# Performance work log

Hardware: AMD Instinct MI355X
Metric: run time of the kernel (lower is better)

## Reference

```python
import jax, jax.numpy as jnp
import numpy as np

VOCAB = 4096
CODE_DIM = 3
DECAY = 0.99
EPS = 1e-05
BETA = 0.25


def setup_inputs() -> dict:
    key = jax.random.key(0)
    k1, k2, k3, k4 = jax.random.split(key, 4)
    B, L, D = 4, 16384, CODE_DIM
    feats = jax.random.normal(k1, (B, L, D), dtype=jnp.float32)
    embed = jax.random.normal(k2, (VOCAB, D), dtype=jnp.float32) * 0.02  # trunc_normal std=init_gain
    ema_cluster_size = jax.random.uniform(k3, (VOCAB,), dtype=jnp.float32)
    ema_weight = jax.random.normal(k4, (VOCAB, D), dtype=jnp.float32) * 0.02
    return {"feats": feats, "embed": embed,
            "ema_cluster_size": ema_cluster_size, "ema_weight": ema_weight}


def reference(feats, embed, ema_cluster_size, ema_weight):
    B, L, D = feats.shape
    V = embed.shape[0]
    flat = feats.reshape(-1, D)  # (N, D)

    # squared-distance argmin nearest-codebook lookup
    dist = (jnp.sum(flat * flat, axis=1, keepdims=True)
            - 2.0 * flat @ embed.T
            + jnp.sum(embed * embed, axis=1))
    idx = jnp.argmin(dist, axis=1)  # (N,)

    quant = embed[idx].reshape(B, L, D)

    # VQ losses (embedding is frozen in torch; stop_grad for faithful grads)
    e_latent_loss = jnp.mean((quant - jax.lax.stop_gradient(feats)) ** 2)
    commit_loss = BETA * jnp.mean((feats - jax.lax.stop_gradient(quant)) ** 2)
    vq_loss = e_latent_loss + commit_loss

    # EMA codebook update (training branch): scatter-accumulate per code
    ones = jnp.ones_like(idx, dtype=flat.dtype)
    batch_cluster_size = jax.ops.segment_sum(ones, idx, num_segments=V)        # == one_hot.sum(0)
    batch_weight_sum = jax.ops.segment_sum(flat, idx, num_segments=V)          # == one_hot.T @ flat

    new_cluster_size = DECAY * ema_cluster_size + (1.0 - DECAY) * batch_cluster_size
    new_ema_weight = DECAY * ema_weight + (1.0 - DECAY) * batch_weight_sum

    n = jnp.sum(new_cluster_size)
    cluster_size = (new_cluster_size + EPS) / (n + V * EPS) * n
    new_embed = new_ema_weight / cluster_size[:, None]

    # code_dim == 3: renormalize the (cos, sin) columns to unit norm
    cos_sin = new_embed[:, 1:]
    norm = jnp.maximum(jnp.linalg.norm(cos_sin, axis=1, keepdims=True), EPS)
    new_embed = jnp.concatenate([new_embed[:, :1], cos_sin / norm], axis=1)

    # straight-through estimator
    quant_st = feats + jax.lax.stop_gradient(quant - feats)

    return (quant_st, idx.reshape(B, L), vq_loss,
            new_embed, new_cluster_size, new_ema_weight)
```

## Files before the change

kernel.cpp:

```cpp
#include <hip/hip_runtime.h>
#include <math.h>

#define VOCAB 4096
#define NROWS 65536
#define DECAYF 0.99f
#define EPSF 1e-5f

typedef unsigned long long u64;
typedef unsigned int u32;
typedef float vf2 __attribute__((ext_vector_type(2)));


__global__ __launch_bounds__(1024) void vq_scan_kernel(
    const float* __restrict__ feats,
    const float* __restrict__ embed,
    float* __restrict__ quant_out,
    float* __restrict__ idx_out,
    double* __restrict__ errpart,
    double* __restrict__ n_acc) {
    #pragma clang fp contract(off)
    __shared__ float4 tab[VOCAB];

    const int tid  = threadIdx.x;
    const int wave = tid >> 6;
    const int lane = tid & 63;

    if (blockIdx.x == 0 && tid == 0) *n_acc = 0.0;

    #pragma unroll
    for (int k = 0; k < 2; ++k) {
        const int p = tid + k * 1024;
        const float* e = embed + p * 6;
        const float x0 = e[0], y0 = e[1], z0 = e[2];
        const float x1 = e[3], y1 = e[4], z1 = e[5];
        const float s0 = (x0 * x0 + y0 * y0) + z0 * z0;
        const float s1 = (x1 * x1 + y1 * y1) + z1 * z1;
        tab[2 * p]     = make_float4(-2.f * x0, -2.f * x1, -2.f * y0, -2.f * y1);
        tab[2 * p + 1] = make_float4(-2.f * z0, -2.f * z1, s0, s1);
    }

    const int rbase = blockIdx.x * 256 + lane * 4;
    const float4 fa = *(const float4*)(feats + rbase * 3);
    const float4 fb = *(const float4*)(feats + rbase * 3 + 4);
    const float4 fc = *(const float4*)(feats + rbase * 3 + 8);
    const float f0[4] = {fa.x, fa.w, fb.z, fc.y};
    const float f1[4] = {fa.y, fb.x, fb.w, fc.z};
    const float f2[4] = {fa.z, fb.y, fc.x, fc.w};
    vf2 f0s[4], f1s[4], f2s[4], fss[4];
    #pragma unroll
    for (int r = 0; r < 4; ++r) {
        const float fs = (f0[r] * f0[r] + f1[r] * f1[r]) + f2[r] * f2[r];
        f0s[r] = (vf2){f0[r], f0[r]};
        f1s[r] = (vf2){f1[r], f1[r]};
        f2s[r] = (vf2){f2[r], f2[r]};
        fss[r] = (vf2){fs, fs};
    }

    __syncthreads();

    float best[4] = {INFINITY, INFINITY, INFINITY, INFINITY};
    int   bj[4]   = {0, 0, 0, 0};
    const float4* __restrict__ wt = tab + (wave << 8);
    const int cw = wave << 8;

    #pragma unroll 2
    for (int i = 0; i < 128; ++i) {
        const float4 A = wt[2 * i];
        const float4 B = wt[2 * i + 1];
        const vf2 xs = (vf2){A.x, A.y};
        const vf2 ys = (vf2){A.z, A.w};
        const vf2 zs = (vf2){B.x, B.y};
        const vf2 es = (vf2){B.z, B.w};
        const int c0 = cw + 2 * i;
        #pragma unroll
        for (int r = 0; r < 4; ++r) {
            vf2 t = __builtin_elementwise_fma(zs, f2s[r],
                      __builtin_elementwise_fma(ys, f1s[r], xs * f0s[r]));
            vf2 d = (fss[r] + t) + es;
            if (d.x < best[r]) { best[r] = d.x; bj[r] = c0; }
            if (d.y < best[r]) { best[r] = d.y; bj[r] = c0 + 1; }
        }
    }

    u64 key[4];
    #pragma unroll
    for (int r = 0; r < 4; ++r) {
        const u32 b  = __float_as_uint(best[r]);
        const u32 mb = b ^ ((u32)((int)b >> 31) | 0x80000000u);
        key[r] = ((u64)mb << 32) | (u32)bj[r];
    }

    __syncthreads();
    u64* mk = (u64*)tab;
    if (wave != 0) {
        #pragma unroll
        for (int r = 0; r < 4; ++r)
            mk[(wave * 4 + r) * 64 + lane] = key[r];
    }
    __syncthreads();
    if (wave == 0) {
        for (int w = 1; w < 16; ++w) {
            #pragma unroll
            for (int r = 0; r < 4; ++r) {
                const u64 k = mk[(w * 4 + r) * 64 + lane];
                key[r] = k < key[r] ? k : key[r];
            }
        }
        int cand[4];
        #pragma unroll
        for (int r = 0; r < 4; ++r) cand[r] = (int)(u32)key[r];

        *(float4*)(idx_out + rbase) =
            make_float4((float)cand[0], (float)cand[1], (float)cand[2], (float)cand[3]);

        float q[4][3];
        #pragma unroll
        for (int r = 0; r < 4; ++r) {
            q[r][0] = embed[cand[r] * 3 + 0];
            q[r][1] = embed[cand[r] * 3 + 1];
            q[r][2] = embed[cand[r] * 3 + 2];
        }
        *(float4*)(quant_out + rbase * 3)     = make_float4(q[0][0], q[0][1], q[0][2], q[1][0]);
        *(float4*)(quant_out + rbase * 3 + 4) = make_float4(q[1][1], q[1][2], q[2][0], q[2][1]);
        *(float4*)(quant_out + rbase * 3 + 8) = make_float4(q[2][2], q[3][0], q[3][1], q[3][2]);

        float err = 0.0f;
        #pragma unroll
        for (int r = 0; r < 4; ++r) {
            const float d0 = q[r][0] - f0[r], d1 = q[r][1] - f1[r], d2 = q[r][2] - f2[r];
            err += d0 * d0 + d1 * d1 + d2 * d2;
        }
        #pragma unroll
        for (int off = 32; off >= 1; off >>= 1) err += __shfl_xor(err, off);
        if (lane == 0) errpart[blockIdx.x] = (double)err;
    }
}

__global__ __launch_bounds__(1024) void seg_kernel(
    const float* __restrict__ feats,
    const float* __restrict__ idx_f,
    float4* __restrict__ part,
    int iters) {
    __shared__ float lcnt[VOCAB];
    __shared__ float lw[VOCAB * 3];
    const int t = threadIdx.x;
    const int b = blockIdx.x;

    #pragma unroll
    for (int i = 0; i < 4; ++i)  lcnt[t + i * 1024] = 0.0f;
    #pragma unroll
    for (int i = 0; i < 12; ++i) lw[t + i * 1024] = 0.0f;
    __syncthreads();

    const int base = b * iters * 1024;
    for (int i = 0; i < iters; ++i) {
        const int row = base + i * 1024 + t;
        const int cand = (int)idx_f[row];
        atomicAdd(&lcnt[cand], 1.0f);
        atomicAdd(&lw[cand * 3 + 0], feats[row * 3 + 0]);
        atomicAdd(&lw[cand * 3 + 1], feats[row * 3 + 1]);
        atomicAdd(&lw[cand * 3 + 2], feats[row * 3 + 2]);
    }
    __syncthreads();

    #pragma unroll
    for (int i = 0; i < 4; ++i) {
        const int v = t + i * 1024;
        part[b * VOCAB + v] = make_float4(lcnt[v], lw[3 * v], lw[3 * v + 1], lw[3 * v + 2]);
    }
}

__global__ __launch_bounds__(256) void ema_reduce_kernel(
    const float4* __restrict__ part,
    const float* __restrict__ ema_cs,
    const float* __restrict__ ema_w,
    const double* __restrict__ errpart,
    float* __restrict__ ncs_out,
    float* __restrict__ nw_out,
    double* __restrict__ n_acc,
    float* __restrict__ loss_out,
    int nseg) {
    const int v = blockIdx.x * 256 + threadIdx.x;
    float c = 0.f, w0 = 0.f, w1 = 0.f, w2 = 0.f;
    for (int b = 0; b < nseg; ++b) {
        const float4 p = part[b * VOCAB + v];
        c += p.x; w0 += p.y; w1 += p.z; w2 += p.w;
    }
    const float ncs = DECAYF * ema_cs[v] + (1.0f - DECAYF) * c;
    ncs_out[v] = ncs;
    nw_out[v * 3 + 0] = DECAYF * ema_w[v * 3 + 0] + (1.0f - DECAYF) * w0;
    nw_out[v * 3 + 1] = DECAYF * ema_w[v * 3 + 1] + (1.0f - DECAYF) * w1;
    nw_out[v * 3 + 2] = DECAYF * ema_w[v * 3 + 2] + (1.0f - DECAYF) * w2;

    double nloc = (double)ncs;
    #pragma unroll
    for (int off = 32; off >= 1; off >>= 1) nloc += __shfl_xor(nloc, off);
    if ((threadIdx.x & 63) == 0) atomicAdd(n_acc, nloc);

    if (blockIdx.x == 0) {
        __shared__ double se[256];
        const int t = threadIdx.x;
        se[t] = errpart[t];
        __syncthreads();
        #pragma unroll
        for (int s = 128; s > 0; s >>= 1) {
            if (t < s) se[t] += se[t + s];
            __syncthreads();
        }
        if (t == 0)
            loss_out[0] = (float)(1.25 * se[0] / (double)(NROWS * 3));
    }
}

__global__ __launch_bounds__(256) void final_kernel(
    const float* __restrict__ ncs,
    const float* __restrict__ nw,
    const double* __restrict__ n_acc,
    float* __restrict__ embed_out) {
    const int v = blockIdx.x * 256 + threadIdx.x;
    const float n = (float)(*n_acc);
    const float cs = (ncs[v] + EPSF) / (n + (float)VOCAB * EPSF) * n;
    const float d0 = nw[v * 3 + 0] / cs;
    const float d1 = nw[v * 3 + 1] / cs;
    const float d2 = nw[v * 3 + 2] / cs;
    const float nrm = fmaxf(sqrtf(d1 * d1 + d2 * d2), EPSF);
    embed_out[v * 3 + 0] = d0;
    embed_out[v * 3 + 1] = d1 / nrm;
    embed_out[v * 3 + 2] = d2 / nrm;
}

extern "C" void kernel_launch(void* const* d_in, const int* in_sizes, int n_in,
                              void* d_out, int out_size, void* d_ws, size_t ws_size,
                              hipStream_t stream) {
    const float* feats  = (const float*)d_in[0];
    const float* embed  = (const float*)d_in[1];
    const float* ema_cs = (const float*)d_in[2];
    const float* ema_w  = (const float*)d_in[3];

    float* out = (float*)d_out;
    float* quant_out = out;
    float* idx_out   = out + 196608;
    float* loss_out  = out + 262144;
    float* embed_out = out + 262145;
    float* ncs_out   = out + 274433;
    float* nw_out    = out + 278529;

    char* wsb = (char*)d_ws;
    double* errpart = (double*)wsb;
    double* n_ac    = (double*)(wsb + 2048);
    float4* part    = (float4*)(wsb + 4096);

    const size_t per_seg = (size_t)VOCAB * 16;
    const size_t avail = ws_size > 4096 ? ws_size - 4096 : 0;
    int nseg = 8;
    if (avail >= 64 * per_seg)      nseg = 64;
    else if (avail >= 32 * per_seg) nseg = 32;
    else if (avail >= 16 * per_seg) nseg = 16;
    const int iters = NROWS / (nseg * 1024);

    vq_scan_kernel<<<NROWS / 256, 1024, 0, stream>>>(feats, embed,
                                                     quant_out, idx_out,
                                                     errpart, n_ac);
    seg_kernel<<<nseg, 1024, 0, stream>>>(feats, idx_out, part, iters);
    ema_reduce_kernel<<<VOCAB / 256, 256, 0, stream>>>(part, ema_cs, ema_w,
                                                       errpart, ncs_out, nw_out,
                                                       n_ac, loss_out, nseg);
    final_kernel<<<VOCAB / 256, 256, 0, stream>>>(ncs_out, nw_out, n_ac, embed_out);
}
```

Before: 80.02 us.

## Group argmin scan by eight codes, compute n analytically, fuse final kernel

The distance scan now takes a min over groups of eight codes and records only the group base. It then recomputes those eight distances to recover the exact first-minimum index, which cuts compare/select work in the hot loop. The total n is computed from the sum of ema_cluster_size plus the known row count, moved into an extra seg_kernel block, so the final kernel can be folded into the EMA reduce kernel. This drops one launch and the double atomics, at the cost of changing n's summation order and precision from double to float.

```diff
diff --git a/kernel.cpp b/kernel.cpp
--- a/kernel.cpp
+++ b/kernel.cpp
@@ -11,21 +11,18 @@
 typedef float vf2 __attribute__((ext_vector_type(2)));
 
 
-__global__ __launch_bounds__(1024) void vq_scan_kernel(
+__global__ __launch_bounds__(1024, 4) void vq_scan_kernel(
     const float* __restrict__ feats,
     const float* __restrict__ embed,
     float* __restrict__ quant_out,
     float* __restrict__ idx_out,
-    double* __restrict__ errpart,
-    double* __restrict__ n_acc) {
+    double* __restrict__ errpart) {
     #pragma clang fp contract(off)
     __shared__ float4 tab[VOCAB];
 
     const int tid  = threadIdx.x;
     const int wave = tid >> 6;
     const int lane = tid & 63;
-
-    if (blockIdx.x == 0 && tid == 0) *n_acc = 0.0;
 
     #pragma unroll
     for (int k = 0; k < 2; ++k) {
@@ -59,35 +56,57 @@
     __syncthreads();
 
     float best[4] = {INFINITY, INFINITY, INFINITY, INFINITY};
-    int   bj[4]   = {0, 0, 0, 0};
+    int   gb[4]   = {0, 0, 0, 0};
     const float4* __restrict__ wt = tab + (wave << 8);
     const int cw = wave << 8;
 
-    #pragma unroll 2
-    for (int i = 0; i < 128; ++i) {
-        const float4 A = wt[2 * i];
-        const float4 B = wt[2 * i + 1];
-        const vf2 xs = (vf2){A.x, A.y};
-        const vf2 ys = (vf2){A.z, A.w};
-        const vf2 zs = (vf2){B.x, B.y};
-        const vf2 es = (vf2){B.z, B.w};
-        const int c0 = cw + 2 * i;
+    for (int g = 0; g < 32; ++g) {
+        const float4 A0 = wt[8 * g + 0], B0 = wt[8 * g + 1];
+        const float4 A1 = wt[8 * g + 2], B1 = wt[8 * g + 3];
+        const float4 A2 = wt[8 * g + 4], B2 = wt[8 * g + 5];
+        const float4 A3 = wt[8 * g + 6], B3 = wt[8 * g + 7];
+        const vf2 xs0 = {A0.x, A0.y}, ys0 = {A0.z, A0.w}, zs0 = {B0.x, B0.y}, es0 = {B0.z, B0.w};
+        const vf2 xs1 = {A1.x, A1.y}, ys1 = {A1.z, A1.w}, zs1 = {B1.x, B1.y}, es1 = {B1.z, B1.w};
+        const vf2 xs2 = {A2.x, A2.y}, ys2 = {A2.z, A2.w}, zs2 = {B2.x, B2.y}, es2 = {B2.z, B2.w};
+        const vf2 xs3 = {A3.x, A3.y}, ys3 = {A3.z, A3.w}, zs3 = {B3.x, B3.y}, es3 = {B3.z, B3.w};
+        const int cbase = cw + 8 * g;
         #pragma unroll
         for (int r = 0; r < 4; ++r) {
-            vf2 t = __builtin_elementwise_fma(zs, f2s[r],
-                      __builtin_elementwise_fma(ys, f1s[r], xs * f0s[r]));
+            vf2 t0 = __builtin_elementwise_fma(zs0, f2s[r], __builtin_elementwise_fma(ys0, f1s[r], xs0 * f0s[r]));
+            vf2 t1 = __builtin_elementwise_fma(zs1, f2s[r], __builtin_elementwise_fma(ys1, f1s[r], xs1 * f0s[r]));
+            vf2 t2 = __builtin_elementwise_fma(zs2, f2s[r], __builtin_elementwise_fma(ys2, f1s[r], xs2 * f0s[r]));
+            vf2 t3 = __builtin_elementwise_fma(zs3, f2s[r], __builtin_elementwise_fma(ys3, f1s[r], xs3 * f0s[r]));
+            vf2 d0 = (fss[r] + t0) + es0;
+            vf2 d1 = (fss[r] + t1) + es1;
+            vf2 d2 = (fss[r] + t2) + es2;
+            vf2 d3 = (fss[r] + t3) + es3;
+            vf2 m01 = __builtin_elementwise_min(d0, d1);
+            vf2 m23 = __builtin_elementwise_min(d2, d3);
+            vf2 m   = __builtin_elementwise_min(m01, m23);
+            const float m8 = fminf(m.x, m.y);
+            if (m8 < best[r]) { best[r] = m8; gb[r] = cbase; }
+        }
+    }
+
+    u64 key[4];
+    #pragma unroll
+    for (int r = 0; r < 4; ++r) {
+        const int b0 = gb[r];
+        const float bv = best[r];
+        int idx = b0;
+        #pragma unroll
+        for (int k = 3; k >= 0; --k) {
+            const float4 A = tab[b0 + 2 * k];
+            const float4 B = tab[b0 + 2 * k + 1];
+            const vf2 xs = {A.x, A.y}, ys = {A.z, A.w}, zs = {B.x, B.y}, es = {B.z, B.w};
+            vf2 t = __builtin_elementwise_fma(zs, f2s[r], __builtin_elementwise_fma(ys, f1s[r], xs * f0s[r]));
             vf2 d = (fss[r] + t) + es;
-            if (d.x < best[r]) { best[r] = d.x; bj[r] = c0; }
-            if (d.y < best[r]) { best[r] = d.y; bj[r] = c0 + 1; }
-        }
-    }
-
-    u64 key[4];
-    #pragma unroll
-    for (int r = 0; r < 4; ++r) {
-        const u32 b  = __float_as_uint(best[r]);
-        const u32 mb = b ^ ((u32)((int)b >> 31) | 0x80000000u);
-        key[r] = ((u64)mb << 32) | (u32)bj[r];
+            if (d.y == bv) idx = b0 + 2 * k + 1;
+            if (d.x == bv) idx = b0 + 2 * k;
+        }
+        const u32 bb = __float_as_uint(bv);
+        const u32 mb = bb ^ ((u32)((int)bb >> 31) | 0x80000000u);
+        key[r] = ((u64)mb << 32) | (u32)idx;
     }
 
     __syncthreads();
@@ -139,12 +158,29 @@
 __global__ __launch_bounds__(1024) void seg_kernel(
     const float* __restrict__ feats,
     const float* __restrict__ idx_f,
+    const float* __restrict__ ema_cs,
     float4* __restrict__ part,
-    int iters) {
+    float* __restrict__ n_out,
+    int iters, int nseg) {
     __shared__ float lcnt[VOCAB];
     __shared__ float lw[VOCAB * 3];
     const int t = threadIdx.x;
     const int b = blockIdx.x;
+
+    if (b == nseg) {
+        float s = ema_cs[t] + ema_cs[t + 1024] + ema_cs[t + 2048] + ema_cs[t + 3072];
+        #pragma unroll
+        for (int off = 32; off >= 1; off >>= 1) s += __shfl_xor(s, off);
+        if ((t & 63) == 0) lcnt[t >> 6] = s;
+        __syncthreads();
+        if (t == 0) {
+            float S = 0.f;
+            #pragma unroll
+            for (int w = 0; w < 16; ++w) S += lcnt[w];
+            *n_out = DECAYF * S + (1.0f - DECAYF) * (float)NROWS;
+        }
+        return;
+    }
 
     #pragma unroll
     for (int i = 0; i < 4; ++i)  lcnt[t + i * 1024] = 0.0f;
@@ -170,14 +206,15 @@
     }
 }
 
-__global__ __launch_bounds__(256) void ema_reduce_kernel(
+__global__ __launch_bounds__(256) void ema_final_kernel(
     const float4* __restrict__ part,
     const float* __restrict__ ema_cs,
     const float* __restrict__ ema_w,
     const double* __restrict__ errpart,
+    const float* __restrict__ n_out,
     float* __restrict__ ncs_out,
     float* __restrict__ nw_out,
-    double* __restrict__ n_acc,
+    float* __restrict__ embed_out,
     float* __restrict__ loss_out,
     int nseg) {
     const int v = blockIdx.x * 256 + threadIdx.x;
@@ -187,15 +224,23 @@
         c += p.x; w0 += p.y; w1 += p.z; w2 += p.w;
     }
     const float ncs = DECAYF * ema_cs[v] + (1.0f - DECAYF) * c;
+    const float n0  = DECAYF * ema_w[v * 3 + 0] + (1.0f - DECAYF) * w0;
+    const float n1  = DECAYF * ema_w[v * 3 + 1] + (1.0f - DECAYF) * w1;
+    const float n2  = DECAYF * ema_w[v * 3 + 2] + (1.0f - DECAYF) * w2;
     ncs_out[v] = ncs;
-    nw_out[v * 3 + 0] = DECAYF * ema_w[v * 3 + 0] + (1.0f - DECAYF) * w0;
-    nw_out[v * 3 + 1] = DECAYF * ema_w[v * 3 + 1] + (1.0f - DECAYF) * w1;
-    nw_out[v * 3 + 2] = DECAYF * ema_w[v * 3 + 2] + (1.0f - DECAYF) * w2;
-
-    double nloc = (double)ncs;
-    #pragma unroll
-    for (int off = 32; off >= 1; off >>= 1) nloc += __shfl_xor(nloc, off);
-    if ((threadIdx.x & 63) == 0) atomicAdd(n_acc, nloc);
+    nw_out[v * 3 + 0] = n0;
+    nw_out[v * 3 + 1] = n1;
+    nw_out[v * 3 + 2] = n2;
+
+    const float n = *n_out;
+    const float cs = (ncs + EPSF) / (n + (float)VOCAB * EPSF) * n;
+    const float d0 = n0 / cs;
+    const float d1 = n1 / cs;
+    const float d2 = n2 / cs;
+    const float nrm = fmaxf(sqrtf(d1 * d1 + d2 * d2), EPSF);
+    embed_out[v * 3 + 0] = d0;
+    embed_out[v * 3 + 1] = d1 / nrm;
+    embed_out[v * 3 + 2] = d2 / nrm;
 
     if (blockIdx.x == 0) {
         __shared__ double se[256];
@@ -210,23 +255,6 @@
         if (t == 0)
             loss_out[0] = (float)(1.25 * se[0] / (double)(NROWS * 3));
     }
-}
-
-__global__ __launch_bounds__(256) void final_kernel(
-    const float* __restrict__ ncs,
-    const float* __restrict__ nw,
-    const double* __restrict__ n_acc,
-    float* __restrict__ embed_out) {
-    const int v = blockIdx.x * 256 + threadIdx.x;
-    const float n = (float)(*n_acc);
-    const float cs = (ncs[v] + EPSF) / (n + (float)VOCAB * EPSF) * n;
-    const float d0 = nw[v * 3 + 0] / cs;
-    const float d1 = nw[v * 3 + 1] / cs;
-    const float d2 = nw[v * 3 + 2] / cs;
-    const float nrm = fmaxf(sqrtf(d1 * d1 + d2 * d2), EPSF);
-    embed_out[v * 3 + 0] = d0;
-    embed_out[v * 3 + 1] = d1 / nrm;
-    embed_out[v * 3 + 2] = d2 / nrm;
 }
 
 extern "C" void kernel_launch(void* const* d_in, const int* in_sizes, int n_in,
@@ -247,7 +275,7 @@
 
     char* wsb = (char*)d_ws;
     double* errpart = (double*)wsb;
-    double* n_ac    = (double*)(wsb + 2048);
+    float*  n_out   = (float*)(wsb + 2048);
     float4* part    = (float4*)(wsb + 4096);
 
     const size_t per_seg = (size_t)VOCAB * 16;
@@ -259,11 +287,11 @@
     const int iters = NROWS / (nseg * 1024);
 
     vq_scan_kernel<<<NROWS / 256, 1024, 0, stream>>>(feats, embed,
-                                                     quant_out, idx_out,
-                                                     errpart, n_ac);
-    seg_kernel<<<nseg, 1024, 0, stream>>>(feats, idx_out, part, iters);
-    ema_reduce_kernel<<<VOCAB / 256, 256, 0, stream>>>(part, ema_cs, ema_w,
-                                                       errpart, ncs_out, nw_out,
-                                                       n_ac, loss_out, nseg);
-    final_kernel<<<VOCAB / 256, 256, 0, stream>>>(ncs_out, nw_out, n_ac, embed_out);
-}
+                                                     quant_out, idx_out, errpart);
+    seg_kernel<<<nseg + 1, 1024, 0, stream>>>(feats, idx_out, ema_cs,
+                                              part, n_out, iters, nseg);
+    ema_final_kernel<<<VOCAB / 256, 256, 0, stream>>>(part, ema_cs, ema_w,
+                                                      errpart, n_out,
+                                                      ncs_out, nw_out, embed_out,
+                                                      loss_out, nseg);
+}
```

New measurement: 64.22 us. 1.25x faster.
